# Kernel tuning notes

Hardware: AMD Instinct MI355X
Metric: run time of the kernel (lower is better)

## Reference

```python
import jax, jax.numpy as jnp
import numpy as np

N_FREQ = 50  # n_frequencies in Model.__init__


def _sine_tables(n_freq):
    i = np.arange(1, n_freq + 1, dtype=np.float32)
    base = 1.0 / (1000.0 ** (2.0 * i / n_freq))           # [n_freq]
    freqs = np.repeat(base, 2)                             # [2*n_freq]
    shifts = np.tile(np.array([0.0, np.pi / 2], dtype=np.float32), n_freq)  # [2*n_freq]
    return jnp.asarray(freqs), jnp.asarray(shifts)


def setup_inputs() -> dict:
    key = jax.random.key(0)
    ks = jax.random.split(key, 8)
    n_frag, n_genes, d_sine, d_emb = 200000, 500, 4 * N_FREQ, 10
    cell_n, gene_n = 200, 500
    coordinates = jax.random.normal(ks[0], (n_frag, 2), dtype=jnp.float32) * 1000.0
    stdv = 1.0 / np.sqrt(d_emb)
    w1 = jax.random.uniform(ks[1], (n_genes, d_sine, d_emb), jnp.float32, -stdv, stdv)
    b1 = jnp.zeros((n_genes, d_emb), jnp.float32)
    w2 = jnp.ones((n_genes, d_emb), jnp.float32)
    b2 = jnp.zeros((n_genes,), jnp.float32)
    genemapping = jax.random.randint(ks[2], (n_frag,), 0, n_genes, dtype=jnp.int64 if jax.config.jax_enable_x64 else jnp.int32)
    local_cellxgene_ix = jax.random.randint(ks[3], (n_frag,), 0, cell_n * gene_n, dtype=genemapping.dtype)
    genes_oi = jnp.arange(gene_n, dtype=genemapping.dtype)
    return {
        "coordinates": coordinates, "w1": w1, "b1": b1, "w2": w2, "b2": b2,
        "genemapping": genemapping, "local_cellxgene_ix": local_cellxgene_ix,
        "genes_oi": genes_oi, "cell_n": cell_n, "gene_n": gene_n,
    }


def reference(coordinates, w1, b1, w2, b2, genemapping, local_cellxgene_ix, genes_oi, cell_n, gene_n):
    freqs, shifts = _sine_tables(N_FREQ)
    n_frag = coordinates.shape[0]
    # SineEncoding: [n_frag, 2, 2*n_freq] -> [n_frag, 4*n_freq]
    emb = jnp.sin(coordinates[..., None] * freqs + shifts).reshape(n_frag, -1)
    # FragmentEmbedder: per-fragment gene-specific linear + sigmoid
    h = jnp.einsum('fs,fsd->fd', emb, w1[genemapping]) + b1[genemapping]
    h = jax.nn.sigmoid(h)
    # EmbeddingGenePooler: scatter-sum into cell x gene bins
    pooled = jax.ops.segment_sum(h, local_cellxgene_ix, num_segments=cell_n * gene_n)
    cge = pooled.reshape(cell_n, gene_n, -1)
    # EmbeddingToExpression: gene-specific dot + bias
    out = (cge * w2[genes_oi]).sum(-1) + b2[genes_oi]
    return out
```

## Files before the change

### kernel.cpp

```cpp
#include <hip/hip_runtime.h>
#include <hip/hip_bf16.h>
#include <math.h>

#define NF    50
#define DEMB  10
#define W1G   (4 * NF * DEMB)
#define MAXG  512

#define HTPB   256
#define HCHUNK 4096
#define HFPT   (HCHUNK / HTPB)

#define HPAD  11
#define TKP   208

typedef __attribute__((ext_vector_type(8))) short short8v;
typedef __attribute__((ext_vector_type(4))) unsigned int uint4v;
typedef __attribute__((ext_vector_type(4))) float f32x4v;

__device__ __forceinline__ short f2bf(float f) {
    union { __hip_bfloat16 b; unsigned short u; } v;
    v.b = __float2bfloat16(f);
    return (short)v.u;
}
__device__ __forceinline__ unsigned pkbf(float lo, float hi) {
    union { __hip_bfloat162 b; unsigned u; } v;
    v.b = __float22bfloat162_rn(make_float2(lo, hi));
    return v.u;
}

__global__ __launch_bounds__(HTPB) void hist_init_k(
    const int* __restrict__ gm, const float* __restrict__ w1,
    short* __restrict__ w1T, int n_frag, int n_genes, int nblk,
    int* __restrict__ counts_mat,
    float* __restrict__ out, const float* __restrict__ b2,
    const int* __restrict__ genes_oi, int gene_n, int total)
{
    __shared__ int lcnt[MAXG];
    __shared__ __align__(16) short tile[DEMB][TKP];

    bool do_hist = (int)blockIdx.x < nblk;
    bool do_tr   = (int)blockIdx.x < n_genes;

    for (int t = threadIdx.x; t < MAXG; t += HTPB) lcnt[t] = 0;
    __syncthreads();

    if (do_hist) {
        int base = blockIdx.x * HCHUNK;
#pragma unroll
        for (int j = 0; j < HFPT; ++j) {
            int f = base + j * HTPB + (int)threadIdx.x;
            if (f < n_frag) atomicAdd(&lcnt[gm[f]], 1);
        }
    }

    if (do_tr) {
        const float* wg = w1 + (size_t)blockIdx.x * W1G;
        for (int e4 = threadIdx.x; e4 < W1G / 4; e4 += HTPB) {
            float4 v = ((const float4*)wg)[e4];
            int e = e4 * 4;
            int k0 = e / 10, d0 = e - k0 * 10;
#pragma unroll
            for (int c = 0; c < 4; ++c) {
                tile[d0][k0] = f2bf((&v.x)[c]);
                d0++; if (d0 == 10) { d0 = 0; k0++; }
            }
        }
    }

    int nthreads = gridDim.x * HTPB;
    for (int i = blockIdx.x * HTPB + (int)threadIdx.x; i < total; i += nthreads) {
        int col = (int)((unsigned)i % (unsigned)gene_n);
        out[i] = b2[genes_oi[col]];
    }
    if (blockIdx.x == 0 && threadIdx.x < 64)
        w1T[(size_t)n_genes * 2000 + threadIdx.x] = 0;

    __syncthreads();

    if (do_hist) {
        int* row = counts_mat + (size_t)blockIdx.x * MAXG;
        for (int t = threadIdx.x; t < MAXG; t += HTPB) row[t] = lcnt[t];
    }
    if (do_tr) {
        short* og = w1T + (size_t)blockIdx.x * 2000;
        for (int o = threadIdx.x; o < 250; o += HTPB) {
            int dd = o / 25;
            int off = (o - dd * 25) * 8;
            *(short8v*)(og + dd * 200 + off) = *(const short8v*)&tile[dd][off];
        }
    }
}

__global__ void scan_k(const int* __restrict__ counts_mat, int nblk,
                       int* __restrict__ po, int* __restrict__ cursor,
                       int* __restrict__ cnt, int* __restrict__ w2g,
                       int* __restrict__ wlim, int n_genes, int wmax)
{
    __shared__ int buf[MAXG];
    int tid = threadIdx.x;
    int s = 0;
#pragma unroll 8
    for (int b = 0; b < nblk; ++b) s += counts_mat[(size_t)b * MAXG + tid];
    int pc = ((s + 63) >> 6) << 6;
    buf[tid] = pc;
    __syncthreads();
    for (int d = 1; d < MAXG; d <<= 1) {
        int t = (tid >= d) ? buf[tid - d] : 0;
        __syncthreads();
        buf[tid] += t;
        __syncthreads();
    }
    int incl = buf[tid];
    if (tid < n_genes) {
        po[tid + 1] = incl;
        cursor[tid] = incl - pc;
        cnt[tid]    = s;
        int wbeg = (incl - pc) >> 6;
        int wend = incl >> 6;
        for (int w = wbeg; w < wend; ++w) {
            w2g[w]  = tid;
            wlim[w] = s - (w - wbeg) * 64;
        }
    }
    if (tid == 0) po[0] = 0;
    __syncthreads();
    int W = buf[n_genes - 1] >> 6;
    for (int w = W + tid; w < wmax; w += MAXG) w2g[w] = -1;
}

__global__ __launch_bounds__(HTPB) void scatter_k(
    const int* __restrict__ gm, const float* __restrict__ coords,
    const int* __restrict__ lcg, int* __restrict__ cursor,
    float* __restrict__ xs, int* __restrict__ bins,
    int n_frag, int n_genes)
{
    __shared__ int lcnt[MAXG];
    __shared__ int lbase[MAXG];
    for (int t = threadIdx.x; t < MAXG; t += HTPB) lcnt[t] = 0;
    __syncthreads();

    int base = blockIdx.x * HCHUNK;
    int g[HFPT], lr[HFPT];
#pragma unroll
    for (int j = 0; j < HFPT; ++j) {
        int f = base + j * HTPB + (int)threadIdx.x;
        if (f < n_frag) {
            g[j]  = gm[f];
            lr[j] = atomicAdd(&lcnt[g[j]], 1);
        } else {
            g[j] = -1;
        }
    }
    __syncthreads();
    for (int t = threadIdx.x; t < MAXG; t += HTPB) {
        int c = lcnt[t];
        lbase[t] = c ? atomicAdd(&cursor[t], c) : 0;
    }
    __syncthreads();
#pragma unroll
    for (int j = 0; j < HFPT; ++j) {
        if (g[j] >= 0) {
            int f = base + j * HTPB + (int)threadIdx.x;
            int pos = lbase[g[j]] + lr[j];
            float2 xy = ((const float2*)coords)[f];
            xs[2 * pos + 0] = xy.x;
            xs[2 * pos + 1] = xy.y;
            bins[pos] = lcg[f];
        }
    }
}

__global__ __launch_bounds__(256, 4) void main_mfma_k(
    const short* __restrict__ w1T, const float* __restrict__ b1,
    const float* __restrict__ w2, const int* __restrict__ genes_oi,
    const float* __restrict__ xs, const int* __restrict__ bins,
    const int* __restrict__ w2g, const int* __restrict__ wlim,
    float* __restrict__ out, int gene_n, int wmax)
{
    __shared__ __align__(16) float fr_ext[116];
    __shared__ __align__(16) float hb_all[4][64 * HPAD];

    if (threadIdx.x < 116) {
        int i = threadIdx.x;
        int im = (i < 50) ? i : ((i < 100) ? i - 50 : i - 100);
        float ex = (-2.0f * (float)(im + 1) / (float)NF) * 9.965784284662087f;
        fr_ext[i] = exp2f(ex) * 0.15915494309189535f;
    }
    __syncthreads();

    int wid  = threadIdx.x >> 6;
    int lane = threadIdx.x & 63;
    int fw   = blockIdx.x * 4 + wid;

    int g   = (fw < wmax) ? w2g[fw]  : -1;
    int lim = (fw < wmax) ? wlim[fw] : 0;
    g = __builtin_amdgcn_readfirstlane(g);
    if (g < 0) return;

    int d  = lane & 15;
    int q  = lane >> 4;
    int dc = (d < 10) ? d : 9;

    bool valid = lane < lim;
    int pos = fw * 64 + lane;

    int bin_own = bins[pos];
    float2 xy_m[4];
#pragma unroll
    for (int m = 0; m < 4; ++m)
        xy_m[m] = ((const float2*)xs)[fw * 64 + m * 16 + d];
    float b1v = b1[(size_t)g * DEMB + dc];
    const short* bp = w1T + (size_t)g * 2000 + dc * 200 + q * 8;
    short8v breg[7];
#pragma unroll
    for (int kk = 0; kk < 7; ++kk)
        breg[kk] = *(const short8v*)(bp + kk * 32);
    __builtin_amdgcn_sched_barrier(0);

    int col_own = (int)((unsigned)bin_own % (unsigned)gene_n);
    int gi = genes_oi[col_own];
    float2 w2v[5];
#pragma unroll
    for (int p2 = 0; p2 < 5; ++p2)
        w2v[p2] = *(const float2*)(w2 + (size_t)gi * DEMB + 2 * p2);
    __builtin_amdgcn_sched_barrier(0);

    f32x4v acc[4];
#pragma unroll
    for (int m = 0; m < 4; ++m) { acc[m][0] = b1v; acc[m][1] = b1v; acc[m][2] = b1v; acc[m][3] = b1v; }

#pragma unroll
    for (int kk = 0; kk < 7; ++kk) {
        float4 fv4 = *(const float4*)&fr_ext[16 * kk + 4 * q];
#pragma unroll
        for (int m = 0; m < 4; ++m) {
            uint4v au;
#pragma unroll
            for (int jj = 0; jj < 4; ++jj) {
                int idx = 16 * kk + 4 * q + jj;
                float fv = (&fv4.x)[jj];
                float xv = (idx < 50) ? xy_m[m].x : xy_m[m].y;
                float r = xv * fv; r -= rintf(r);
                au[jj] = pkbf(__builtin_amdgcn_sinf(r), __builtin_amdgcn_cosf(r));
            }
            if (kk == 6 && q > 0) {
                au[0] = 0; au[1] = 0; au[2] = 0; au[3] = 0;
            }
            short8v afrag = __builtin_bit_cast(short8v, au);
            acc[m] = __builtin_amdgcn_mfma_f32_16x16x32_bf16(afrag, breg[kk], acc[m], 0, 0, 0);
        }
    }

    float* hb = hb_all[wid];
    if (d < 10) {
#pragma unroll
        for (int m = 0; m < 4; ++m)
#pragma unroll
            for (int r = 0; r < 4; ++r)
                hb[(m * 16 + q * 4 + r) * HPAD + d] = acc[m][r];
    }

    float sum = 0.0f;
#pragma unroll
    for (int p2 = 0; p2 < 5; ++p2) {
        float h0 = hb[lane * HPAD + 2 * p2];
        float h1 = hb[lane * HPAD + 2 * p2 + 1];
        sum += w2v[p2].x / (1.0f + __expf(-h0));
        sum += w2v[p2].y / (1.0f + __expf(-h1));
    }
    if (valid) atomicAdd(&out[bin_own], sum);
}

__global__ __launch_bounds__(256) void frag_naive_k(
    const float* __restrict__ coords, const float* __restrict__ w1,
    const float* __restrict__ b1, const float* __restrict__ w2,
    const int* __restrict__ gm, const int* __restrict__ lcg,
    const int* __restrict__ genes_oi, float* __restrict__ out,
    int gene_n, int n_frag)
{
    __shared__ float fr[NF];
    if (threadIdx.x < NF) {
        float ex = (-2.0f * (float)(threadIdx.x + 1) / (float)NF) * 9.965784284662087f;
        fr[threadIdx.x] = exp2f(ex) * 0.15915494309189535f;
    }
    __syncthreads();

    int f = blockIdx.x * blockDim.x + threadIdx.x;
    if (f >= n_frag) return;
    int g = gm[f];
    const float* wrow  = w1 + (size_t)g * W1G;
    const float* b1row = b1 + (size_t)g * DEMB;
    float x0 = coords[2 * f + 0];
    float x1 = coords[2 * f + 1];

    float h[DEMB];
#pragma unroll
    for (int d = 0; d < DEMB; ++d) h[d] = b1row[d];
#pragma unroll 2
    for (int i = 0; i < NF; ++i) {
        float fv = fr[i];
        float r0 = x0 * fv; r0 -= rintf(r0);
        float r1 = x1 * fv; r1 -= rintf(r1);
        float s0 = __builtin_amdgcn_sinf(r0), c0 = __builtin_amdgcn_cosf(r0);
        float s1 = __builtin_amdgcn_sinf(r1), c1 = __builtin_amdgcn_cosf(r1);
        const float* wa = wrow + (2 * i) * DEMB;
        const float* wb = wrow + (2 * NF + 2 * i) * DEMB;
#pragma unroll
        for (int d = 0; d < DEMB; ++d) {
            h[d] += s0 * wa[d] + c0 * wa[DEMB + d] + s1 * wb[d] + c1 * wb[DEMB + d];
        }
    }
    int bin = lcg[f];
    int col = (int)((unsigned)bin % (unsigned)gene_n);
    const float* w2row = w2 + (size_t)genes_oi[col] * DEMB;
    float sum = 0.0f;
#pragma unroll
    for (int d = 0; d < DEMB; ++d) {
        float sg = 1.0f / (1.0f + __expf(-h[d]));
        sum += sg * w2row[d];
    }
    atomicAdd(&out[bin], sum);
}

__global__ void init_out_k(float* __restrict__ out, const float* __restrict__ b2,
                           const int* __restrict__ genes_oi, int gene_n, int total)
{
    int i = blockIdx.x * blockDim.x + threadIdx.x;
    if (i < total) {
        int col = (int)((unsigned)i % (unsigned)gene_n);
        out[i] = b2[genes_oi[col]];
    }
}

extern "C" void kernel_launch(void* const* d_in, const int* in_sizes, int n_in,
                              void* d_out, int out_size, void* d_ws, size_t ws_size,
                              hipStream_t stream)
{
    const float* coords   = (const float*)d_in[0];
    const float* w1       = (const float*)d_in[1];
    const float* b1       = (const float*)d_in[2];
    const float* w2       = (const float*)d_in[3];
    const float* b2       = (const float*)d_in[4];
    const int*   gm       = (const int*)d_in[5];
    const int*   lcg      = (const int*)d_in[6];
    const int*   genes_oi = (const int*)d_in[7];

    int n_frag  = in_sizes[5];
    int n_genes = in_sizes[4];
    int gene_n  = in_sizes[7];
    int total   = out_size;
    float* out  = (float*)d_out;

    int nblk = (n_frag + HCHUNK - 1) / HCHUNK;
    int wmax = (n_frag >> 6) + n_genes + 1;
    size_t padcap = (size_t)n_frag + 64 * (size_t)n_genes + 64;

    short* w1T      = (short*)d_ws;
    size_t w1T_sh   = (size_t)n_genes * 2000 + 64;
    if (w1T_sh & 1) ++w1T_sh;
    int* counts_mat = (int*)(w1T + w1T_sh);
    int* po         = counts_mat + (size_t)nblk * MAXG;
    int* cursor     = po + (MAXG + 1);
    int* cnt        = cursor + MAXG;
    int* w2g        = cnt + MAXG;
    int* wlim       = w2g + wmax;
    float* xs       = (float*)(wlim + wmax);
    int* bins       = (int*)(xs + 2 * padcap);
    size_t need = w1T_sh * sizeof(short)
                + ((size_t)nblk * MAXG + (MAXG + 1) + 2 * MAXG + 2 * (size_t)wmax
                   + 3 * padcap) * sizeof(int);

    bool use_sorted = (ws_size >= need) && (n_genes <= MAXG);
    if (use_sorted) {
        int g1 = (nblk > n_genes) ? nblk : n_genes;
        hist_init_k<<<g1, HTPB, 0, stream>>>(gm, w1, w1T, n_frag, n_genes, nblk,
                                             counts_mat, out, b2, genes_oi, gene_n, total);
        scan_k<<<1, MAXG, 0, stream>>>(counts_mat, nblk, po, cursor, cnt, w2g,
                                       wlim, n_genes, wmax);
        scatter_k<<<nblk, HTPB, 0, stream>>>(gm, coords, lcg, cursor,
                                             xs, bins, n_frag, n_genes);
        int mblk = (wmax + 3) / 4;
        main_mfma_k<<<mblk, 256, 0, stream>>>(w1T, b1, w2, genes_oi, xs, bins,
                                              w2g, wlim, out, gene_n, wmax);
    } else {
        init_out_k<<<(total + 255) / 256, 256, 0, stream>>>(out, b2, genes_oi, gene_n, total);
        frag_naive_k<<<(n_frag + 255) / 256, 256, 0, stream>>>(coords, w1, b1, w2, gm, lcg,
                                                               genes_oi, out, gene_n, n_frag);
    }
}
```

Baseline: 45.34 us.

## Fuse scan into histogram kernel via last-block ticket, stage gene weights in LDS

Removes the separate single-block scan launch: the last block to finish the histogram/transpose kernel (found with an atomic ticket counter) performs the prefix scan. Gene segments are now padded to 256 fragments so each main-kernel block serves a single gene. That block loads the bf16 weight tile once into shared memory instead of each wave reading it from global memory. This saves a launch and redundant weight loads, at the cost of more padding and a hipMemsetAsync for the ticket counter. The scan now runs serially on one block at the tail of the first kernel.

```diff
diff --git a/kernel.cpp b/kernel.cpp
--- a/kernel.cpp
+++ b/kernel.cpp
@@ -29,34 +29,39 @@
     return v.u;
 }
 
-__global__ __launch_bounds__(HTPB) void hist_init_k(
+__global__ __launch_bounds__(HTPB) void hist_scan_k(
     const int* __restrict__ gm, const float* __restrict__ w1,
     short* __restrict__ w1T, int n_frag, int n_genes, int nblk,
-    int* __restrict__ counts_mat,
-    float* __restrict__ out, const float* __restrict__ b2,
-    const int* __restrict__ genes_oi, int gene_n, int total)
+    int* __restrict__ counts_mat, float* __restrict__ out,
+    const float* __restrict__ b2, const int* __restrict__ genes_oi,
+    int gene_n, int total, int* __restrict__ done,
+    int* __restrict__ cursor, int4* __restrict__ blk_info, int bmax)
 {
     __shared__ int lcnt[MAXG];
     __shared__ __align__(16) short tile[DEMB][TKP];
-
-    bool do_hist = (int)blockIdx.x < nblk;
-    bool do_tr   = (int)blockIdx.x < n_genes;
-
-    for (int t = threadIdx.x; t < MAXG; t += HTPB) lcnt[t] = 0;
+    __shared__ int sbuf[MAXG];
+    __shared__ int ticket_s;
+
+    const int tid = threadIdx.x;
+    const int bid = blockIdx.x;
+
+    bool do_hist = bid < nblk;
+    bool do_tr   = bid < n_genes;
+
+    for (int t = tid; t < MAXG; t += HTPB) lcnt[t] = 0;
     __syncthreads();
 
     if (do_hist) {
-        int base = blockIdx.x * HCHUNK;
+        int base = bid * HCHUNK;
 #pragma unroll
         for (int j = 0; j < HFPT; ++j) {
-            int f = base + j * HTPB + (int)threadIdx.x;
+            int f = base + j * HTPB + tid;
             if (f < n_frag) atomicAdd(&lcnt[gm[f]], 1);
         }
     }
-
     if (do_tr) {
-        const float* wg = w1 + (size_t)blockIdx.x * W1G;
-        for (int e4 = threadIdx.x; e4 < W1G / 4; e4 += HTPB) {
+        const float* wg = w1 + (size_t)bid * W1G;
+        for (int e4 = tid; e4 < W1G / 4; e4 += HTPB) {
             float4 v = ((const float4*)wg)[e4];
             int e = e4 * 4;
             int k0 = e / 10, d0 = e - k0 * 10;
@@ -69,64 +74,74 @@
     }
 
     int nthreads = gridDim.x * HTPB;
-    for (int i = blockIdx.x * HTPB + (int)threadIdx.x; i < total; i += nthreads) {
+    for (int i = bid * HTPB + tid; i < total; i += nthreads) {
         int col = (int)((unsigned)i % (unsigned)gene_n);
         out[i] = b2[genes_oi[col]];
     }
-    if (blockIdx.x == 0 && threadIdx.x < 64)
-        w1T[(size_t)n_genes * 2000 + threadIdx.x] = 0;
+    if (bid == 0 && tid < 64) w1T[(size_t)n_genes * 2000 + tid] = 0;
 
     __syncthreads();
 
     if (do_hist) {
-        int* row = counts_mat + (size_t)blockIdx.x * MAXG;
-        for (int t = threadIdx.x; t < MAXG; t += HTPB) row[t] = lcnt[t];
+        int* row = counts_mat + (size_t)bid * MAXG;
+        for (int t = tid; t < MAXG; t += HTPB) row[t] = lcnt[t];
     }
     if (do_tr) {
-        short* og = w1T + (size_t)blockIdx.x * 2000;
-        for (int o = threadIdx.x; o < 250; o += HTPB) {
+        short* og = w1T + (size_t)bid * 2000;
+        for (int o = tid; o < 250; o += HTPB) {
             int dd = o / 25;
             int off = (o - dd * 25) * 8;
             *(short8v*)(og + dd * 200 + off) = *(const short8v*)&tile[dd][off];
         }
     }
-}
-
-__global__ void scan_k(const int* __restrict__ counts_mat, int nblk,
-                       int* __restrict__ po, int* __restrict__ cursor,
-                       int* __restrict__ cnt, int* __restrict__ w2g,
-                       int* __restrict__ wlim, int n_genes, int wmax)
-{
-    __shared__ int buf[MAXG];
-    int tid = threadIdx.x;
-    int s = 0;
-#pragma unroll 8
-    for (int b = 0; b < nblk; ++b) s += counts_mat[(size_t)b * MAXG + tid];
-    int pc = ((s + 63) >> 6) << 6;
-    buf[tid] = pc;
-    __syncthreads();
-    for (int d = 1; d < MAXG; d <<= 1) {
-        int t = (tid >= d) ? buf[tid - d] : 0;
+
+    __threadfence();
+    if (tid == 0) ticket_s = atomicAdd(done, 1);
+    __syncthreads();
+    if (ticket_s != (int)gridDim.x - 1) return;
+    __threadfence();
+
+    int i0 = tid, i1 = tid + 256;
+    int s0 = 0, s1 = 0;
+    for (int b = 0; b < nblk; ++b) {
+        const int* row = counts_mat + (size_t)b * MAXG;
+        s0 += row[i0]; s1 += row[i1];
+    }
+    int pc0 = ((s0 + 255) >> 8) << 8;
+    int pc1 = ((s1 + 255) >> 8) << 8;
+    sbuf[i0] = pc0; sbuf[i1] = pc1;
+    __syncthreads();
+    for (int ds = 1; ds < MAXG; ds <<= 1) {
+        int t0 = (i0 >= ds) ? sbuf[i0 - ds] : 0;
+        int t1 = (i1 >= ds) ? sbuf[i1 - ds] : 0;
         __syncthreads();
-        buf[tid] += t;
+        sbuf[i0] += t0; sbuf[i1] += t1;
         __syncthreads();
     }
-    int incl = buf[tid];
-    if (tid < n_genes) {
-        po[tid + 1] = incl;
-        cursor[tid] = incl - pc;
-        cnt[tid]    = s;
-        int wbeg = (incl - pc) >> 6;
-        int wend = incl >> 6;
-        for (int w = wbeg; w < wend; ++w) {
-            w2g[w]  = tid;
-            wlim[w] = s - (w - wbeg) * 64;
-        }
-    }
-    if (tid == 0) po[0] = 0;
-    __syncthreads();
-    int W = buf[n_genes - 1] >> 6;
-    for (int w = W + tid; w < wmax; w += MAXG) w2g[w] = -1;
+    if (i0 < n_genes) {
+        int incl = sbuf[i0];
+        int start = incl - pc0;
+        cursor[i0] = start;
+        int nb = pc0 >> 8;
+        for (int j = 0; j < nb; ++j) {
+            int lim = s0 - j * 256; lim = (lim < 256) ? lim : 256;
+            blk_info[(start >> 8) + j] = make_int4(i0, start + j * 256, lim, 0);
+        }
+    }
+    if (i1 < n_genes) {
+        int incl = sbuf[i1];
+        int start = incl - pc1;
+        cursor[i1] = start;
+        int nb = pc1 >> 8;
+        for (int j = 0; j < nb; ++j) {
+            int lim = s1 - j * 256; lim = (lim < 256) ? lim : 256;
+            blk_info[(start >> 8) + j] = make_int4(i1, start + j * 256, lim, 0);
+        }
+    }
+    __syncthreads();
+    int Bt = sbuf[n_genes - 1] >> 8;
+    for (int b = Bt + tid; b < bmax; b += HTPB)
+        blk_info[b] = make_int4(-1, 0, 0, 0);
 }
 
 __global__ __launch_bounds__(HTPB) void scatter_k(
@@ -175,48 +190,51 @@
     const short* __restrict__ w1T, const float* __restrict__ b1,
     const float* __restrict__ w2, const int* __restrict__ genes_oi,
     const float* __restrict__ xs, const int* __restrict__ bins,
-    const int* __restrict__ w2g, const int* __restrict__ wlim,
-    float* __restrict__ out, int gene_n, int wmax)
-{
+    const int4* __restrict__ blk_info, float* __restrict__ out,
+    int gene_n)
+{
+    __shared__ __align__(16) short Bs[2048];
     __shared__ __align__(16) float fr_ext[116];
     __shared__ __align__(16) float hb_all[4][64 * HPAD];
 
-    if (threadIdx.x < 116) {
-        int i = threadIdx.x;
+    int4 bi = blk_info[blockIdx.x];
+    int g = bi.x;
+    if (g < 0) return;
+    int start = bi.y;
+    int lim   = bi.z;
+
+    const int tid = threadIdx.x;
+
+    if (tid < 250) {
+        *(short8v*)&Bs[tid * 8] = *(const short8v*)(w1T + (size_t)g * 2000 + tid * 8);
+    } else {
+        *(short8v*)&Bs[2000 + (tid - 250) * 8] = (short8v)0;
+    }
+    if (tid < 116) {
+        int i = tid;
         int im = (i < 50) ? i : ((i < 100) ? i - 50 : i - 100);
         float ex = (-2.0f * (float)(im + 1) / (float)NF) * 9.965784284662087f;
         fr_ext[i] = exp2f(ex) * 0.15915494309189535f;
     }
     __syncthreads();
 
-    int wid  = threadIdx.x >> 6;
-    int lane = threadIdx.x & 63;
-    int fw   = blockIdx.x * 4 + wid;
-
-    int g   = (fw < wmax) ? w2g[fw]  : -1;
-    int lim = (fw < wmax) ? wlim[fw] : 0;
-    g = __builtin_amdgcn_readfirstlane(g);
-    if (g < 0) return;
+    int wid  = tid >> 6;
+    int lane = tid & 63;
+    if (wid * 64 >= lim) return;
 
     int d  = lane & 15;
     int q  = lane >> 4;
     int dc = (d < 10) ? d : 9;
 
-    bool valid = lane < lim;
-    int pos = fw * 64 + lane;
+    bool valid = (wid * 64 + lane) < lim;
+    int pos = start + wid * 64 + lane;
 
     int bin_own = bins[pos];
     float2 xy_m[4];
 #pragma unroll
     for (int m = 0; m < 4; ++m)
-        xy_m[m] = ((const float2*)xs)[fw * 64 + m * 16 + d];
+        xy_m[m] = ((const float2*)xs)[start + wid * 64 + m * 16 + d];
     float b1v = b1[(size_t)g * DEMB + dc];
-    const short* bp = w1T + (size_t)g * 2000 + dc * 200 + q * 8;
-    short8v breg[7];
-#pragma unroll
-    for (int kk = 0; kk < 7; ++kk)
-        breg[kk] = *(const short8v*)(bp + kk * 32);
-    __builtin_amdgcn_sched_barrier(0);
 
     int col_own = (int)((unsigned)bin_own % (unsigned)gene_n);
     int gi = genes_oi[col_own];
@@ -224,7 +242,12 @@
 #pragma unroll
     for (int p2 = 0; p2 < 5; ++p2)
         w2v[p2] = *(const float2*)(w2 + (size_t)gi * DEMB + 2 * p2);
-    __builtin_amdgcn_sched_barrier(0);
+
+    const short* bp = Bs + dc * 200 + q * 8;
+    short8v breg[7];
+#pragma unroll
+    for (int kk = 0; kk < 7; ++kk)
+        breg[kk] = *(const short8v*)(bp + kk * 32);
 
     f32x4v acc[4];
 #pragma unroll
@@ -353,36 +376,30 @@
     float* out  = (float*)d_out;
 
     int nblk = (n_frag + HCHUNK - 1) / HCHUNK;
-    int wmax = (n_frag >> 6) + n_genes + 1;
-    size_t padcap = (size_t)n_frag + 64 * (size_t)n_genes + 64;
-
-    short* w1T      = (short*)d_ws;
-    size_t w1T_sh   = (size_t)n_genes * 2000 + 64;
-    if (w1T_sh & 1) ++w1T_sh;
-    int* counts_mat = (int*)(w1T + w1T_sh);
-    int* po         = counts_mat + (size_t)nblk * MAXG;
-    int* cursor     = po + (MAXG + 1);
-    int* cnt        = cursor + MAXG;
-    int* w2g        = cnt + MAXG;
-    int* wlim       = w2g + wmax;
-    float* xs       = (float*)(wlim + wmax);
-    int* bins       = (int*)(xs + 2 * padcap);
-    size_t need = w1T_sh * sizeof(short)
-                + ((size_t)nblk * MAXG + (MAXG + 1) + 2 * MAXG + 2 * (size_t)wmax
-                   + 3 * padcap) * sizeof(int);
+    int bmax = (n_frag >> 8) + n_genes + 1;
+    size_t padcap = (size_t)n_frag + 256 * (size_t)n_genes + 256;
+
+    char* p = (char*)d_ws;
+    short* w1T = (short*)p;                 p += (((size_t)n_genes * 2000 + 64) * 2 + 15) / 16 * 16;
+    int4* blk_info = (int4*)p;              p += (size_t)bmax * 16;
+    int* counts_mat = (int*)p;              p += (size_t)nblk * MAXG * 4;
+    int* cursor = (int*)p;                  p += MAXG * 4;
+    int* done = (int*)p;                    p += 16;
+    float* xs = (float*)p;                  p += padcap * 2 * 4;
+    int* bins = (int*)p;                    p += padcap * 4;
+    size_t need = (size_t)(p - (char*)d_ws);
 
     bool use_sorted = (ws_size >= need) && (n_genes <= MAXG);
     if (use_sorted) {
+        hipMemsetAsync(done, 0, sizeof(int), stream);
         int g1 = (nblk > n_genes) ? nblk : n_genes;
-        hist_init_k<<<g1, HTPB, 0, stream>>>(gm, w1, w1T, n_frag, n_genes, nblk,
-                                             counts_mat, out, b2, genes_oi, gene_n, total);
-        scan_k<<<1, MAXG, 0, stream>>>(counts_mat, nblk, po, cursor, cnt, w2g,
-                                       wlim, n_genes, wmax);
+        hist_scan_k<<<g1, HTPB, 0, stream>>>(gm, w1, w1T, n_frag, n_genes, nblk,
+                                             counts_mat, out, b2, genes_oi, gene_n,
+                                             total, done, cursor, blk_info, bmax);
         scatter_k<<<nblk, HTPB, 0, stream>>>(gm, coords, lcg, cursor,
                                              xs, bins, n_frag, n_genes);
-        int mblk = (wmax + 3) / 4;
-        main_mfma_k<<<mblk, 256, 0, stream>>>(w1T, b1, w2, genes_oi, xs, bins,
-                                              w2g, wlim, out, gene_n, wmax);
+        main_mfma_k<<<bmax, 256, 0, stream>>>(w1T, b1, w2, genes_oi, xs, bins,
+                                              blk_info, out, gene_n);
     } else {
         init_out_k<<<(total + 255) / 256, 256, 0, stream>>>(out, b2, genes_oi, gene_n, total);
         frag_naive_k<<<(n_frag + 255) / 256, 256, 0, stream>>>(coords, w1, b1, w2, gm, lcg,
```

Result: slower. 96.86 us (+113.6%).
